# Performance work log

Hardware: AMD Instinct MI355X
Metric: run time of the kernel (lower is better)

Reference implementation:

```python
import jax, jax.numpy as jnp
import numpy as np

FT = 0.2  # clip floor (init arg ft)

def _norm_mat(m):
    # matrix / (count of nonzeros along last dim + 1e-30)
    deg = jnp.sum(m != 0, axis=-1, keepdims=True).astype(m.dtype)
    return m / (deg + 1e-30)

def _l2n(x):
    return x / (jnp.linalg.norm(x, axis=-1, keepdims=True) + 1e-30)

def setup_inputs():
    B, L, D, H, O = 2, 2048, 64, 64, 128
    N = 2 * L
    ks = jax.random.split(jax.random.key(0), 30)
    u = lambda i, s: jax.random.uniform(ks[i], s, jnp.float32)
    g = lambda i, s: jax.random.normal(ks[i], s, jnp.float32) * 0.05
    inp = {}
    inp['word_outputs_0'] = g(0, (B, L, D))
    inp['word_outputs_1'] = g(1, (B, L, D))
    inp['node_hidden'] = g(2, (B, D))
    inp['op_embedding'] = g(3, (B, O, D))
    inp['word_exist_sequence'] = (u(4, (B, N)) < 0.8).astype(jnp.float32)
    inp['word_exist_matrix'] = (u(5, (B, N, N)) < 0.8).astype(jnp.float32)
    inp['word_operator'] = (u(6, (B, N, O)) < 0.02).astype(jnp.float32)
    inp['word_word'] = (u(7, (B, N, N)) < 0.01).astype(jnp.float32)
    inp['depend_0'] = (u(8, (B, L, L)) < 0.05).astype(jnp.float32)
    inp['depend_1'] = (u(9, (B, L, L)) < 0.05).astype(jnp.float32)
    inp['goal_word'] = u(10, (B, N))
    names = [('Wg', (D, H)), ('bg', (H,)), ('Wwk', (D, H)), ('bwk', (H,)),
             ('Wws', (D, H)), ('bws', (H,)), ('Wo', (D, D)), ('bo', (D,)),
             ('Wupd', (3 * H, D)), ('bupd', (D,)), ('Wf', (3 * H + D, D)), ('bf', (D,)),
             ('Wf2', (2 * D, D)), ('bf2', (D,)), ('Wout', (D, D)), ('bout', (D,))]
    for i, (nm, s) in enumerate(names):
        inp[nm] = g(11 + i, s)
    return inp

def _forward(w0, w1, nh, opE, wes, wem, wop, ww, d0, d1, gw,
             Wg, bg, Wwk, bwk, Wws, bws, Wo, bo, Wupd, bupd, Wf, bf, Wf2, bf2, Wout, bout):
    all_w = jnp.concatenate([w0, w1], axis=1)                      # [B,N,D]
    goal_trans = (nh @ Wg + bg)[:, None, :]                        # [B,1,H] (broadcast = expand)
    word_g = _l2n(goal_trans * gw[..., None])                      # [B,N,H]
    word_w_k = _l2n(jnp.matmul(_norm_mat(ww * wem), all_w @ Wwk + bwk))
    ws0 = jnp.matmul(_norm_mat(d0), w0 @ Wws + bws)
    ws1 = jnp.matmul(_norm_mat(d1), w1 @ Wws + bws)
    word_w_s = _l2n(jnp.concatenate([ws0, ws1], axis=1))           # [B,N,H]
    neigh = jnp.concatenate([word_g, word_w_k, word_w_s], axis=-1)  # [B,N,3H]
    forget = jax.nn.sigmoid(jnp.concatenate([all_w, word_g, word_w_k, word_w_s], axis=-1) @ Wf + bf)
    word_updated = jnp.maximum(forget, FT) * all_w + (1.0 - forget) * jax.nn.relu(neigh @ Wupd + bupd)
    adj_op = _norm_mat(jnp.swapaxes(wes[..., None] * wop, 1, 2))   # [B,O,N]
    word_op = jnp.matmul(adj_op, word_updated @ Wo + bo)           # [B,O,D]
    forget2 = jax.nn.sigmoid(jnp.concatenate([opE, word_op], axis=-1) @ Wf2 + bf2)
    op_out = jnp.maximum(forget2, FT) * opE + (1.0 - forget2) * jax.nn.relu(word_op @ Wout + bout)
    # original returns (split(word_updated), op_embedding); concat along node axis here
    return jnp.concatenate([word_updated, op_out], axis=1)         # [B,N+O,D]

def reference(word_outputs_0, word_outputs_1, node_hidden, op_embedding,
              word_exist_sequence, word_exist_matrix, word_operator, word_word,
              depend_0, depend_1, goal_word,
              Wg, bg, Wwk, bwk, Wws, bws, Wo, bo, Wupd, bupd, Wf, bf, Wf2, bf2, Wout, bout):
    return _forward(word_outputs_0, word_outputs_1, node_hidden, op_embedding,
                    word_exist_sequence, word_exist_matrix, word_operator, word_word,
                    depend_0, depend_1, goal_word,
                    Wg, bg, Wwk, bwk, Wws, bws, Wo, bo, Wupd, bupd, Wf, bf, Wf2, bf2, Wout, bout)
```

## Files before the change

### kernel.cpp

```cpp
#include <hip/hip_runtime.h>
#include <cstdint>

typedef unsigned short u16;
typedef unsigned long long u64;

__device__ __forceinline__ float b2f(u16 u){
  union { uint32_t i; float f; } v; v.i = ((uint32_t)u) << 16; return v.f;
}
__device__ __forceinline__ u16 f2b(float f){
  union { float f; uint32_t i; } v; v.f = f;
  uint32_t r = v.i + 0x7FFFu + ((v.i >> 16) & 1u);
  return (u16)(r >> 16);
}
__device__ __forceinline__ float sigmoidf(float x){ return 1.0f / (1.0f + __expf(-x)); }
__device__ __forceinline__ uint32_t slot(uint4 v, int s){
  return (s==0) ? v.x : (s==1) ? v.y : (s==2) ? v.z : v.w;
}

__global__ void k_pre(const float* __restrict__ nh, const float* __restrict__ Wg,
                      const float* __restrict__ bg, float* __restrict__ ghat){
  int b = threadIdx.x >> 6, h = threadIdx.x & 63;
  float g = bg[h];
  for (int d = 0; d < 64; ++d) g += nh[b*64 + d] * Wg[d*64 + h];
  float ss = g * g;
  #pragma unroll
  for (int o = 32; o > 0; o >>= 1) ss += __shfl_xor(ss, o, 64);
  ghat[b*64 + h] = g / (sqrtf(ss) + 1e-30f);
}

__global__ __launch_bounds__(256) void k_xform(
    const float* __restrict__ w0, const float* __restrict__ w1,
    const float* __restrict__ Wwk, const float* __restrict__ bwk,
    const float* __restrict__ Wws, const float* __restrict__ bws,
    float* __restrict__ Xk, float* __restrict__ Xs){
  __shared__ float sWk[4096], sWs[4096];
  int tid = threadIdx.x;
  for (int i = tid; i < 1024; i += 256){
    ((float4*)sWk)[i] = ((const float4*)Wwk)[i];
    ((float4*)sWs)[i] = ((const float4*)Wws)[i];
  }
  __syncthreads();
  int lane = tid & 63, wave = tid >> 6;
  float bk = bwk[lane], bs = bws[lane];
  float aw[4];
  #pragma unroll
  for (int t = 0; t < 4; ++t){
    int row = blockIdx.x*4 + wave + t*2048;
    int b = row >> 12, n = row & 4095;
    aw[t] = (n < 2048) ? w0[((size_t)(b*2048 + n))*64 + lane]
                       : w1[((size_t)(b*2048 + n - 2048))*64 + lane];
  }
  #pragma unroll
  for (int t = 0; t < 4; ++t){
    int row = blockIdx.x*4 + wave + t*2048;
    float xk = bk, xs = bs;
    #pragma unroll 8
    for (int d = 0; d < 64; ++d){
      float a = __shfl(aw[t], d, 64);
      xk += a * sWk[d*64 + lane];
      xs += a * sWs[d*64 + lane];
    }
    Xk[(size_t)row*64 + lane] = xk;
    Xs[(size_t)row*64 + lane] = xs;
  }
}

template<bool TWO, int WPR>
__global__ __launch_bounds__(256) void k_maskmean(
    const float* __restrict__ mA, const float* __restrict__ mB,
    const float* __restrict__ X, float* __restrict__ outp,
    int rows, int cols, int xB, int xoff, int outB){
  __shared__ int q[4][1024];
  __shared__ float sacc[4][64];
  __shared__ int scnt[4];
  constexpr int RPB = 4 / WPR;
  int lane = threadIdx.x & 63, wave = threadIdx.x >> 6;
  int wir = wave & (WPR - 1), sub = wave / WPR;
  int rr = blockIdx.x * RPB + sub;
  int b = rr / rows, r = rr - b*rows;
  size_t base = ((size_t)b*rows + r) * cols + (size_t)wir*1024;
  const float* Xb = X + (size_t)b*xB + (size_t)xoff*64 + lane;
  uint4 av[4], bv[4];
  #pragma unroll
  for (int c = 0; c < 4; ++c){
    av[c] = ((const uint4*)(mA + base))[c*64 + lane];
    if (TWO) bv[c] = ((const uint4*)(mB + base))[c*64 + lane];
  }
  u64 lt = (1ULL << lane) - 1ULL;
  int cnt = 0;
  #pragma unroll
  for (int c = 0; c < 4; ++c){
    #pragma unroll
    for (int s = 0; s < 4; ++s){
      bool nz = (slot(av[c], s) & 0x7fffffffu) != 0;
      if (TWO) nz = nz && ((slot(bv[c], s) & 0x7fffffffu) != 0);
      u64 m = __ballot(nz);
      if (nz) q[wave][cnt + (int)__popcll(m & lt)] = wir*1024 + c*256 + lane*4 + s;
      cnt += (int)__popcll(m);
    }
  }
  float acc = 0.f;
  int i = 0;
  for (; i + 8 <= cnt; i += 8){
    int4 c0 = *(const int4*)&q[wave][i];
    int4 c1 = *(const int4*)&q[wave][i + 4];
    float v0 = Xb[(size_t)c0.x*64], v1 = Xb[(size_t)c0.y*64];
    float v2 = Xb[(size_t)c0.z*64], v3 = Xb[(size_t)c0.w*64];
    float v4 = Xb[(size_t)c1.x*64], v5 = Xb[(size_t)c1.y*64];
    float v6 = Xb[(size_t)c1.z*64], v7 = Xb[(size_t)c1.w*64];
    acc += ((v0 + v1) + (v2 + v3)) + ((v4 + v5) + (v6 + v7));
  }
  for (; i < cnt; ++i) acc += Xb[(size_t)q[wave][i]*64];
  sacc[wave][lane] = acc;
  if (lane == 0) scnt[wave] = cnt;
  __syncthreads();
  if (wir == 0){
    float t = 0.f; int dg = 0;
    #pragma unroll
    for (int j = 0; j < WPR; ++j){ t += sacc[sub*WPR + j][lane]; dg += scnt[sub*WPR + j]; }
    float mean = t / ((float)dg + 1e-30f);
    float ss = mean * mean;
    #pragma unroll
    for (int o = 32; o > 0; o >>= 1) ss += __shfl_xor(ss, o, 64);
    outp[(size_t)b*outB + (size_t)r*64 + lane] = mean / (sqrtf(ss) + 1e-30f);
  }
}

__global__ __launch_bounds__(256, 2) void k_update(
    const float* __restrict__ w0, const float* __restrict__ w1,
    const float* __restrict__ gw, const float* __restrict__ ghat,
    const float* __restrict__ wwkn, const float* __restrict__ wwsn,
    const float* __restrict__ Wf, const float* __restrict__ bf,
    const float* __restrict__ Wupd, const float* __restrict__ bupd,
    float* __restrict__ out, float* __restrict__ WU){
  __shared__ uint32_t pWf[128*64];
  __shared__ uint32_t pWu[96*64];
  __shared__ float xsh[4][256];
  int tid = threadIdx.x;
  for (int i = tid; i < 8192; i += 256){
    int k2 = i >> 6, ln = i & 63;
    pWf[i] = (uint32_t)f2b(Wf[(2*k2)*64 + ln]) | ((uint32_t)f2b(Wf[(2*k2+1)*64 + ln]) << 16);
  }
  for (int i = tid; i < 6144; i += 256){
    int k2 = i >> 6, ln = i & 63;
    pWu[i] = (uint32_t)f2b(Wupd[(2*k2)*64 + ln]) | ((uint32_t)f2b(Wupd[(2*k2+1)*64 + ln]) << 16);
  }
  __syncthreads();
  int lane = tid & 63, wave = tid >> 6;
  float bff = bf[lane], bup = bupd[lane];
  float aw[4], wgv[4], wk[4], wsv[4];
  #pragma unroll
  for (int t = 0; t < 4; ++t){
    int row = blockIdx.x*4 + wave + t*2048;
    int b = row >> 12, n = row & 4095;
    aw[t] = (n < 2048) ? w0[((size_t)(b*2048 + n))*64 + lane]
                       : w1[((size_t)(b*2048 + n - 2048))*64 + lane];
    float gvv = gw[b*4096 + n];
    wgv[t] = (gvv != 0.f) ? ghat[b*64 + lane] : 0.f;
    wk[t]  = wwkn[(size_t)row*64 + lane];
    wsv[t] = wwsn[(size_t)row*64 + lane];
  }
  #pragma unroll
  for (int t = 0; t < 4; ++t){
    int row = blockIdx.x*4 + wave + t*2048;
    int b = row >> 12, n = row & 4095;
    xsh[wave][lane] = aw[t]; xsh[wave][64 + lane] = wgv[t];
    xsh[wave][128 + lane] = wk[t]; xsh[wave][192 + lane] = wsv[t];
    float f = bff, u = bup;
    #pragma unroll 8
    for (int k2 = 0; k2 < 32; ++k2){
      float2 xv = *(const float2*)&xsh[wave][2*k2];
      uint32_t wf = pWf[k2*64 + lane];
      f += xv.x * b2f((u16)wf) + xv.y * b2f((u16)(wf >> 16));
    }
    #pragma unroll 8
    for (int k2 = 32; k2 < 128; ++k2){
      float2 xv = *(const float2*)&xsh[wave][2*k2];
      uint32_t wf = pWf[k2*64 + lane];
      uint32_t wu = pWu[(k2 - 32)*64 + lane];
      f += xv.x * b2f((u16)wf) + xv.y * b2f((u16)(wf >> 16));
      u += xv.x * b2f((u16)wu) + xv.y * b2f((u16)(wu >> 16));
    }
    f = sigmoidf(f);
    u = fmaxf(u, 0.f);
    float wu = fmaxf(f, 0.2f) * aw[t] + (1.f - f) * u;
    out[((size_t)b*4224 + n)*64 + lane] = wu;
    WU[(size_t)row*64 + lane] = wu;
  }
}

__global__ __launch_bounds__(256) void k_wuo(
    const float* __restrict__ WU, const float* __restrict__ Wo,
    const float* __restrict__ bo, float* __restrict__ WUo){
  __shared__ float sWo[4096];
  int tid = threadIdx.x;
  for (int i = tid; i < 1024; i += 256) ((float4*)sWo)[i] = ((const float4*)Wo)[i];
  __syncthreads();
  int lane = tid & 63, wave = tid >> 6;
  float boo = bo[lane];
  float wu[4];
  #pragma unroll
  for (int t = 0; t < 4; ++t){
    int row = blockIdx.x*4 + wave + t*2048;
    wu[t] = WU[(size_t)row*64 + lane];
  }
  #pragma unroll
  for (int t = 0; t < 4; ++t){
    int row = blockIdx.x*4 + wave + t*2048;
    float o = boo;
    #pragma unroll 8
    for (int d = 0; d < 64; ++d) o += __shfl(wu[t], d, 64) * sWo[d*64 + lane];
    WUo[(size_t)row*64 + lane] = o;
  }
}

__global__ __launch_bounds__(256) void k_opagg(
    const float* __restrict__ wes, const float* __restrict__ wop,
    const float* __restrict__ WUo, float* __restrict__ wordop){
  __shared__ int q[4][1024];
  __shared__ float sacc[4][64];
  __shared__ int scnt[4];
  int blk = blockIdx.x;
  int b = blk >> 7, o = blk & 127;
  int lane = threadIdx.x & 63, wave = threadIdx.x >> 6;
  const float* wesb = wes + b*4096 + wave*1024;
  const float* Xb = WUo + (size_t)b*4096*64 + lane;
  uint4 av[4]; float wv[16];
  #pragma unroll
  for (int c = 0; c < 4; ++c) av[c] = ((const uint4*)wesb)[c*64 + lane];
  #pragma unroll
  for (int c = 0; c < 4; ++c)
    #pragma unroll
    for (int s = 0; s < 4; ++s)
      wv[c*4 + s] = wop[(size_t)(b*4096 + wave*1024 + c*256 + lane*4 + s)*128 + o];
  u64 lt = (1ULL << lane) - 1ULL;
  int cnt = 0;
  #pragma unroll
  for (int c = 0; c < 4; ++c){
    #pragma unroll
    for (int s = 0; s < 4; ++s){
      bool nz = ((slot(av[c], s) & 0x7fffffffu) != 0) && (wv[c*4 + s] != 0.f);
      u64 m = __ballot(nz);
      if (nz) q[wave][cnt + (int)__popcll(m & lt)] = wave*1024 + c*256 + lane*4 + s;
      cnt += (int)__popcll(m);
    }
  }
  float acc = 0.f;
  int i = 0;
  for (; i + 8 <= cnt; i += 8){
    int4 c0 = *(const int4*)&q[wave][i];
    int4 c1 = *(const int4*)&q[wave][i + 4];
    float v0 = Xb[(size_t)c0.x*64], v1 = Xb[(size_t)c0.y*64];
    float v2 = Xb[(size_t)c0.z*64], v3 = Xb[(size_t)c0.w*64];
    float v4 = Xb[(size_t)c1.x*64], v5 = Xb[(size_t)c1.y*64];
    float v6 = Xb[(size_t)c1.z*64], v7 = Xb[(size_t)c1.w*64];
    acc += ((v0 + v1) + (v2 + v3)) + ((v4 + v5) + (v6 + v7));
  }
  for (; i < cnt; ++i) acc += Xb[(size_t)q[wave][i]*64];
  sacc[wave][lane] = acc;
  if (lane == 0) scnt[wave] = cnt;
  __syncthreads();
  if (wave == 0){
    float t = sacc[0][lane] + sacc[1][lane] + sacc[2][lane] + sacc[3][lane];
    float deg = (float)(scnt[0] + scnt[1] + scnt[2] + scnt[3]);
    wordop[(size_t)blk*64 + lane] = t / (deg + 1e-30f);
  }
}

__global__ __launch_bounds__(256) void k_opout(
    const float* __restrict__ opE, const float* __restrict__ wordop,
    const float* __restrict__ Wf2, const float* __restrict__ bf2,
    const float* __restrict__ Wout, const float* __restrict__ bout,
    float* __restrict__ out){
  __shared__ float sW2[8192];
  __shared__ float sWo[4096];
  __shared__ float xsh[4][128];
  int tid = threadIdx.x;
  for (int i = tid; i < 2048; i += 256) ((float4*)sW2)[i] = ((const float4*)Wf2)[i];
  for (int i = tid; i < 1024; i += 256) ((float4*)sWo)[i] = ((const float4*)Wout)[i];
  __syncthreads();
  int lane = tid & 63, wave = tid >> 6;
  int row = blockIdx.x*4 + wave;
  int b = row >> 7, o = row & 127;
  float e  = opE[(size_t)row*64 + lane];
  float wo = wordop[(size_t)row*64 + lane];
  xsh[wave][lane] = e; xsh[wave][64 + lane] = wo;
  float f = bf2[lane], u = bout[lane];
  #pragma unroll 8
  for (int k = 0; k < 128; ++k) f += xsh[wave][k] * sW2[k*64 + lane];
  #pragma unroll 8
  for (int d = 0; d < 64; ++d)  u += xsh[wave][64 + d] * sWo[d*64 + lane];
  f = sigmoidf(f);
  u = fmaxf(u, 0.f);
  float res = fmaxf(f, 0.2f) * e + (1.f - f) * u;
  out[((size_t)b*4224 + 4096 + o)*64 + lane] = res;
}

extern "C" void kernel_launch(void* const* d_in, const int* in_sizes, int n_in,
                              void* d_out, int out_size, void* d_ws, size_t ws_size,
                              hipStream_t stream){
  const float* w0   = (const float*)d_in[0];
  const float* w1   = (const float*)d_in[1];
  const float* nh   = (const float*)d_in[2];
  const float* opE  = (const float*)d_in[3];
  const float* wes  = (const float*)d_in[4];
  const float* wem  = (const float*)d_in[5];
  const float* wop  = (const float*)d_in[6];
  const float* ww   = (const float*)d_in[7];
  const float* d0   = (const float*)d_in[8];
  const float* d1   = (const float*)d_in[9];
  const float* gw   = (const float*)d_in[10];
  const float* Wg   = (const float*)d_in[11];
  const float* bg   = (const float*)d_in[12];
  const float* Wwk  = (const float*)d_in[13];
  const float* bwk  = (const float*)d_in[14];
  const float* Wws  = (const float*)d_in[15];
  const float* bws  = (const float*)d_in[16];
  const float* Wo   = (const float*)d_in[17];
  const float* bo   = (const float*)d_in[18];
  const float* Wupd = (const float*)d_in[19];
  const float* bupd = (const float*)d_in[20];
  const float* Wf   = (const float*)d_in[21];
  const float* bf   = (const float*)d_in[22];
  const float* Wf2  = (const float*)d_in[23];
  const float* bf2  = (const float*)d_in[24];
  const float* Wout = (const float*)d_in[25];
  const float* bout = (const float*)d_in[26];

  float* ws   = (float*)d_ws;
  float* ghat = ws;
  float* Xk   = ghat + 128;
  float* Xs   = Xk + 524288;
  float* wwkn = Xs + 524288;
  float* wwsn = wwkn + 524288;
  float* wopm = wwsn + 524288;
  float* WU   = Xk;
  float* WUo  = Xs;
  float* out  = (float*)d_out;

  k_pre<<<1, 128, 0, stream>>>(nh, Wg, bg, ghat);
  k_xform<<<512, 256, 0, stream>>>(w0, w1, Wwk, bwk, Wws, bws, Xk, Xs);
  k_maskmean<true , 4><<<8192, 256, 0, stream>>>(ww, wem, Xk, wwkn, 4096, 4096, 4096*64, 0,    4096*64);
  k_maskmean<false, 2><<<2048, 256, 0, stream>>>(d0, nullptr, Xs, wwsn,           2048, 2048, 4096*64, 0,    4096*64);
  k_maskmean<false, 2><<<2048, 256, 0, stream>>>(d1, nullptr, Xs, wwsn + 2048*64, 2048, 2048, 4096*64, 2048, 4096*64);
  k_update<<<512, 256, 0, stream>>>(w0, w1, gw, ghat, wwkn, wwsn, Wf, bf, Wupd, bupd, out, WU);
  k_wuo<<<512, 256, 0, stream>>>(WU, Wo, bo, WUo);
  k_opagg<<<256, 256, 0, stream>>>(wes, wop, WUo, wopm);
  k_opout<<<64, 256, 0, stream>>>(opE, wopm, Wf2, bf2, Wout, bout, out);
}
```

Before: 454.2 us.

## Replace sparse gather mask-mean with dense bf16 MFMA split-K matmul

The ballot/compaction plus gather mask-mean kernels are replaced by a dense matmul. Mask nonzeros become bf16 ones and are multiplied by a transposed bf16 copy of the transformed features using MFMA 16x16x32 instructions, with double-buffered LDS staging, split-K and atomicAdd reduction. A separate kernel then L2-normalizes the sums, which removes the need to divide by the degree. The intent is to turn latency-bound irregular gathers into a streaming, tensor-core-friendly pass. The cost is bf16 rounding of the features, extra transpose and memset launches, and atomic traffic.

```diff
diff --git a/kernel.cpp b/kernel.cpp
--- a/kernel.cpp
+++ b/kernel.cpp
@@ -3,18 +3,20 @@
 
 typedef unsigned short u16;
 typedef unsigned long long u64;
-
-__device__ __forceinline__ float b2f(u16 u){
-  union { uint32_t i; float f; } v; v.i = ((uint32_t)u) << 16; return v.f;
-}
+typedef __attribute__((ext_vector_type(8))) short bf16x8;
+typedef __attribute__((ext_vector_type(4))) float f32x4;
+
 __device__ __forceinline__ u16 f2b(float f){
   union { float f; uint32_t i; } v; v.f = f;
   uint32_t r = v.i + 0x7FFFu + ((v.i >> 16) & 1u);
   return (u16)(r >> 16);
 }
+__device__ __forceinline__ float b2f(u16 u){
+  union { uint32_t i; float f; } v; v.i = ((uint32_t)u) << 16; return v.f;
+}
 __device__ __forceinline__ float sigmoidf(float x){ return 1.0f / (1.0f + __expf(-x)); }
-__device__ __forceinline__ uint32_t slot(uint4 v, int s){
-  return (s==0) ? v.x : (s==1) ? v.y : (s==2) ? v.z : v.w;
+__device__ __forceinline__ uint32_t nzb(float a){
+  return (__float_as_uint(a) << 1) ? 0x3F80u : 0u;
 }
 
 __global__ void k_pre(const float* __restrict__ nh, const float* __restrict__ Wg,
@@ -65,65 +67,123 @@
   }
 }
 
-template<bool TWO, int WPR>
-__global__ __launch_bounds__(256) void k_maskmean(
-    const float* __restrict__ mA, const float* __restrict__ mB,
-    const float* __restrict__ X, float* __restrict__ outp,
-    int rows, int cols, int xB, int xoff, int outB){
-  __shared__ int q[4][1024];
-  __shared__ float sacc[4][64];
-  __shared__ int scnt[4];
-  constexpr int RPB = 4 / WPR;
-  int lane = threadIdx.x & 63, wave = threadIdx.x >> 6;
-  int wir = wave & (WPR - 1), sub = wave / WPR;
-  int rr = blockIdx.x * RPB + sub;
-  int b = rr / rows, r = rr - b*rows;
-  size_t base = ((size_t)b*rows + r) * cols + (size_t)wir*1024;
-  const float* Xb = X + (size_t)b*xB + (size_t)xoff*64 + lane;
-  uint4 av[4], bv[4];
+__global__ __launch_bounds__(256) void k_tr(const float* __restrict__ src, u16* __restrict__ dst){
+  __shared__ u16 sm[64][65];
+  int tile = blockIdx.x;
+  int b = tile >> 6, n0 = (tile & 63) * 64;
+  int tid = threadIdx.x;
+  int r = tid >> 2, seg = (tid & 3) * 16;
+  const float* s = src + ((size_t)b*4096 + n0 + r) * 64 + seg;
   #pragma unroll
   for (int c = 0; c < 4; ++c){
-    av[c] = ((const uint4*)(mA + base))[c*64 + lane];
-    if (TWO) bv[c] = ((const uint4*)(mB + base))[c*64 + lane];
-  }
-  u64 lt = (1ULL << lane) - 1ULL;
-  int cnt = 0;
-  #pragma unroll
-  for (int c = 0; c < 4; ++c){
+    float4 v = ((const float4*)s)[c];
+    sm[r][seg + c*4 + 0] = f2b(v.x);
+    sm[r][seg + c*4 + 1] = f2b(v.y);
+    sm[r][seg + c*4 + 2] = f2b(v.z);
+    sm[r][seg + c*4 + 3] = f2b(v.w);
+  }
+  __syncthreads();
+  int d = tid >> 2, ns = (tid & 3) * 16;
+  u16* o = dst + (size_t)b*64*4096 + (size_t)d*4096 + n0 + ns;
+  #pragma unroll
+  for (int j = 0; j < 8; ++j){
+    uint32_t lo = sm[ns + 2*j][d], hi = sm[ns + 2*j + 1][d];
+    ((uint32_t*)o)[j] = lo | (hi << 16);
+  }
+}
+
+template<bool TWO>
+__global__ __launch_bounds__(256) void k_mm(
+    const float* __restrict__ M1, const float* __restrict__ M2,
+    const u16* __restrict__ XT, float* __restrict__ sums,
+    int rowsPB, int cols, int numRT, int kspan, int xoff){
+  __shared__ u16 Bm[2][64*72];
+  __shared__ u16 Ax[2][64*72];
+  int rt = blockIdx.x % numRT;
+  int ks = blockIdx.x / numRT;
+  int rr0 = rt * 64;
+  int b = rr0 / rowsPB, r0 = rr0 % rowsPB;
+  int k0 = ks * kspan;
+  int tid = threadIdx.x;
+  int rsub = tid >> 2, seg = tid & 3, kk = seg * 16;
+  const float* m1t = M1 + ((size_t)b*rowsPB + r0 + rsub) * cols + k0 + kk;
+  const float* m2t = TWO ? (M2 + ((size_t)b*rowsPB + r0 + rsub) * cols + k0 + kk) : nullptr;
+  const u16*   xtt = XT + (size_t)b*64*4096 + (size_t)rsub*4096 + xoff + k0 + kk;
+  int lane = tid & 63, w = tid >> 6, quad = lane >> 4, l15 = lane & 15;
+
+  f32x4 acc[4] = {f32x4{0,0,0,0}, f32x4{0,0,0,0}, f32x4{0,0,0,0}, f32x4{0,0,0,0}};
+  int niter = kspan >> 6;
+
+  float4 am0, am1, am2, am3, bn0, bn1, bn2, bn3;
+  uint4 x0, x1;
+
+#define ISSUE(IT) do{ size_t off = (size_t)(IT) * 64;                         \
+    am0 = ((const float4*)(m1t + off))[0]; am1 = ((const float4*)(m1t + off))[1]; \
+    am2 = ((const float4*)(m1t + off))[2]; am3 = ((const float4*)(m1t + off))[3]; \
+    if (TWO){                                                                  \
+      bn0 = ((const float4*)(m2t + off))[0]; bn1 = ((const float4*)(m2t + off))[1]; \
+      bn2 = ((const float4*)(m2t + off))[2]; bn3 = ((const float4*)(m2t + off))[3]; \
+    }                                                                          \
+    x0 = ((const uint4*)(xtt + off))[0]; x1 = ((const uint4*)(xtt + off))[1]; }while(0)
+
+#define PK(a, bb) (TWO ? ((nzb(a.x) && nzb(bb.x) ? 0x3F80u : 0u) | ((nzb(a.y) && nzb(bb.y) ? 0x3F80u : 0u) << 16)) \
+                       : (nzb(a.x) | (nzb(a.y) << 16)))
+#define PK2(a, bb) (TWO ? ((nzb(a.z) && nzb(bb.z) ? 0x3F80u : 0u) | ((nzb(a.w) && nzb(bb.w) ? 0x3F80u : 0u) << 16)) \
+                        : (nzb(a.z) | (nzb(a.w) << 16)))
+
+#define COMMIT(BUF) do{                                                        \
+    uint4 pa, pb;                                                              \
+    pa.x = PK(am0, bn0); pa.y = PK2(am0, bn0); pa.z = PK(am1, bn1); pa.w = PK2(am1, bn1); \
+    pb.x = PK(am2, bn2); pb.y = PK2(am2, bn2); pb.z = PK(am3, bn3); pb.w = PK2(am3, bn3); \
+    *(uint4*)&Bm[BUF][rsub*72 + kk]     = pa;                                  \
+    *(uint4*)&Bm[BUF][rsub*72 + kk + 8] = pb;                                  \
+    *(uint4*)&Ax[BUF][rsub*72 + kk]     = x0;                                  \
+    *(uint4*)&Ax[BUF][rsub*72 + kk + 8] = x1; }while(0)
+
+  ISSUE(0);
+  COMMIT(0);
+  __syncthreads();
+  for (int it = 0; it < niter; ++it){
+    int buf = it & 1;
+    if (it + 1 < niter) ISSUE(it + 1);
     #pragma unroll
-    for (int s = 0; s < 4; ++s){
-      bool nz = (slot(av[c], s) & 0x7fffffffu) != 0;
-      if (TWO) nz = nz && ((slot(bv[c], s) & 0x7fffffffu) != 0);
-      u64 m = __ballot(nz);
-      if (nz) q[wave][cnt + (int)__popcll(m & lt)] = wir*1024 + c*256 + lane*4 + s;
-      cnt += (int)__popcll(m);
+    for (int s = 0; s < 2; ++s){
+      int ko = s*32 + quad*8;
+      bf16x8 bfr = *(const bf16x8*)&Bm[buf][(w*16 + l15)*72 + ko];
+      #pragma unroll
+      for (int m = 0; m < 4; ++m){
+        bf16x8 afr = *(const bf16x8*)&Ax[buf][(m*16 + l15)*72 + ko];
+        acc[m] = __builtin_amdgcn_mfma_f32_16x16x32_bf16(afr, bfr, acc[m], 0, 0, 0);
+      }
     }
-  }
-  float acc = 0.f;
-  int i = 0;
-  for (; i + 8 <= cnt; i += 8){
-    int4 c0 = *(const int4*)&q[wave][i];
-    int4 c1 = *(const int4*)&q[wave][i + 4];
-    float v0 = Xb[(size_t)c0.x*64], v1 = Xb[(size_t)c0.y*64];
-    float v2 = Xb[(size_t)c0.z*64], v3 = Xb[(size_t)c0.w*64];
-    float v4 = Xb[(size_t)c1.x*64], v5 = Xb[(size_t)c1.y*64];
-    float v6 = Xb[(size_t)c1.z*64], v7 = Xb[(size_t)c1.w*64];
-    acc += ((v0 + v1) + (v2 + v3)) + ((v4 + v5) + (v6 + v7));
-  }
-  for (; i < cnt; ++i) acc += Xb[(size_t)q[wave][i]*64];
-  sacc[wave][lane] = acc;
-  if (lane == 0) scnt[wave] = cnt;
-  __syncthreads();
-  if (wir == 0){
-    float t = 0.f; int dg = 0;
+    if (it + 1 < niter) COMMIT((it + 1) & 1);
+    __syncthreads();
+  }
+  float* od = sums + (size_t)(b*4096 + xoff + r0 + w*16 + l15) * 64;
+  #pragma unroll
+  for (int m = 0; m < 4; ++m)
     #pragma unroll
-    for (int j = 0; j < WPR; ++j){ t += sacc[sub*WPR + j][lane]; dg += scnt[sub*WPR + j]; }
-    float mean = t / ((float)dg + 1e-30f);
-    float ss = mean * mean;
-    #pragma unroll
-    for (int o = 32; o > 0; o >>= 1) ss += __shfl_xor(ss, o, 64);
-    outp[(size_t)b*outB + (size_t)r*64 + lane] = mean / (sqrtf(ss) + 1e-30f);
-  }
+    for (int g = 0; g < 4; ++g)
+      atomicAdd(&od[m*16 + quad*4 + g], acc[m][g]);
+#undef ISSUE
+#undef COMMIT
+#undef PK
+#undef PK2
+}
+
+__global__ __launch_bounds__(256) void k_norm(
+    const float* __restrict__ sb, const float* __restrict__ sd,
+    float* __restrict__ wwkn, float* __restrict__ wwsn){
+  int idx = blockIdx.x*4 + (threadIdx.x >> 6);
+  int lane = threadIdx.x & 63;
+  const float* s; float* d;
+  if (idx < 8192){ s = sb + (size_t)idx*64; d = wwkn + (size_t)idx*64; }
+  else           { s = sd + (size_t)(idx - 8192)*64; d = wwsn + (size_t)(idx - 8192)*64; }
+  float v = s[lane];
+  float ss = v * v;
+  #pragma unroll
+  for (int o = 32; o > 0; o >>= 1) ss += __shfl_xor(ss, o, 64);
+  d[lane] = v / (sqrtf(ss) + 1e-30f);
 }
 
 __global__ __launch_bounds__(256, 2) void k_update(
@@ -239,7 +299,8 @@
   for (int c = 0; c < 4; ++c){
     #pragma unroll
     for (int s = 0; s < 4; ++s){
-      bool nz = ((slot(av[c], s) & 0x7fffffffu) != 0) && (wv[c*4 + s] != 0.f);
+      uint32_t wa = (s==0)?av[c].x:(s==1)?av[c].y:(s==2)?av[c].z:av[c].w;
+      bool nz = ((wa & 0x7fffffffu) != 0) && (wv[c*4 + s] != 0.f);
       u64 m = __ballot(nz);
       if (nz) q[wave][cnt + (int)__popcll(m & lt)] = wave*1024 + c*256 + lane*4 + s;
       cnt += (int)__popcll(m);
@@ -334,15 +395,24 @@
   float* wwkn = Xs + 524288;
   float* wwsn = wwkn + 524288;
   float* wopm = wwsn + 524288;
+  u16*  XkT   = (u16*)(wopm + 16384);
+  u16*  XsT   = (u16*)(wopm + 16384 + 262144);
+  float* sums_big = Xk;
+  float* sums_dep = Xs;
   float* WU   = Xk;
   float* WUo  = Xs;
   float* out  = (float*)d_out;
 
   k_pre<<<1, 128, 0, stream>>>(nh, Wg, bg, ghat);
   k_xform<<<512, 256, 0, stream>>>(w0, w1, Wwk, bwk, Wws, bws, Xk, Xs);
-  k_maskmean<true , 4><<<8192, 256, 0, stream>>>(ww, wem, Xk, wwkn, 4096, 4096, 4096*64, 0,    4096*64);
-  k_maskmean<false, 2><<<2048, 256, 0, stream>>>(d0, nullptr, Xs, wwsn,           2048, 2048, 4096*64, 0,    4096*64);
-  k_maskmean<false, 2><<<2048, 256, 0, stream>>>(d1, nullptr, Xs, wwsn + 2048*64, 2048, 2048, 4096*64, 2048, 4096*64);
+  k_tr<<<128, 256, 0, stream>>>(Xk, XkT);
+  k_tr<<<128, 256, 0, stream>>>(Xs, XsT);
+  hipMemsetAsync(sums_big, 0, 524288 * sizeof(float), stream);
+  hipMemsetAsync(sums_dep, 0, 524288 * sizeof(float), stream);
+  k_mm<true ><<<1024, 256, 0, stream>>>(ww, wem, XkT, sums_big, 4096, 4096, 128, 512, 0);
+  k_mm<false><<<256, 256, 0, stream>>>(d0, nullptr, XsT, sums_dep, 2048, 2048, 64, 512, 0);
+  k_mm<false><<<256, 256, 0, stream>>>(d1, nullptr, XsT, sums_dep, 2048, 2048, 64, 512, 2048);
+  k_norm<<<4096, 256, 0, stream>>>(sums_big, sums_dep, wwkn, wwsn);
   k_update<<<512, 256, 0, stream>>>(w0, w1, gw, ghat, wwkn, wwsn, Wf, bf, Wupd, bupd, out, WU);
   k_wuo<<<512, 256, 0, stream>>>(WU, Wo, bo, WUo);
   k_opagg<<<256, 256, 0, stream>>>(wes, wop, WUo, wopm);
```

Result: slower. 519.8 us (+14.5%).

## Precompute adjacency bitmasks, then gather with prefix-sum compaction and bf16 outputs

Applied to the files above, without the earlier changes.

The fused mask-and-mean kernels are split in two. A streaming pass packs each adjacency row, and the word-operator mask, into 64-bit bitmasks via ballots. A second pass expands the set bits with a wave prefix-sum into index lists and gathers the transformed rows. The operator aggregation reads compact per-node bitmasks instead of striding down the word_operator column, which is meant to remove heavily uncoalesced reads. The normalized neighbour means are now stored as bf16, which lowers precision and adds extra kernel launches and bitmask traffic.

```diff
diff --git a/kernel.cpp b/kernel.cpp
--- a/kernel.cpp
+++ b/kernel.cpp
@@ -4,18 +4,15 @@
 typedef unsigned short u16;
 typedef unsigned long long u64;
 
-__device__ __forceinline__ float b2f(u16 u){
-  union { uint32_t i; float f; } v; v.i = ((uint32_t)u) << 16; return v.f;
-}
 __device__ __forceinline__ u16 f2b(float f){
   union { float f; uint32_t i; } v; v.f = f;
   uint32_t r = v.i + 0x7FFFu + ((v.i >> 16) & 1u);
   return (u16)(r >> 16);
 }
+__device__ __forceinline__ float b2f(u16 u){
+  union { uint32_t i; float f; } v; v.i = ((uint32_t)u) << 16; return v.f;
+}
 __device__ __forceinline__ float sigmoidf(float x){ return 1.0f / (1.0f + __expf(-x)); }
-__device__ __forceinline__ uint32_t slot(uint4 v, int s){
-  return (s==0) ? v.x : (s==1) ? v.y : (s==2) ? v.z : v.w;
-}
 
 __global__ void k_pre(const float* __restrict__ nh, const float* __restrict__ Wg,
                       const float* __restrict__ bg, float* __restrict__ ghat){
@@ -65,43 +62,77 @@
   }
 }
 
-template<bool TWO, int WPR>
-__global__ __launch_bounds__(256) void k_maskmean(
-    const float* __restrict__ mA, const float* __restrict__ mB,
-    const float* __restrict__ X, float* __restrict__ outp,
-    int rows, int cols, int xB, int xoff, int outB){
-  __shared__ int q[4][1024];
-  __shared__ float sacc[4][64];
-  __shared__ int scnt[4];
-  constexpr int RPB = 4 / WPR;
+template<bool TWO, int JS>
+__global__ __launch_bounds__(256) void k_bits(
+    const float* __restrict__ A, const float* __restrict__ B, u64* __restrict__ bits){
   int lane = threadIdx.x & 63, wave = threadIdx.x >> 6;
-  int wir = wave & (WPR - 1), sub = wave / WPR;
-  int rr = blockIdx.x * RPB + sub;
-  int b = rr / rows, r = rr - b*rows;
-  size_t base = ((size_t)b*rows + r) * cols + (size_t)wir*1024;
-  const float* Xb = X + (size_t)b*xB + (size_t)xoff*64 + lane;
-  uint4 av[4], bv[4];
-  #pragma unroll
-  for (int c = 0; c < 4; ++c){
-    av[c] = ((const uint4*)(mA + base))[c*64 + lane];
-    if (TWO) bv[c] = ((const uint4*)(mB + base))[c*64 + lane];
-  }
-  u64 lt = (1ULL << lane) - 1ULL;
-  int cnt = 0;
-  #pragma unroll
-  for (int c = 0; c < 4; ++c){
+  int row = blockIdx.x*4 + wave;
+  const float* a = A + (size_t)row * (JS*256) + lane*4;
+  const float* bb = TWO ? (B + (size_t)row * (JS*256) + lane*4) : nullptr;
+  u64 myword = 0;
+  #pragma unroll 4
+  for (int j = 0; j < JS; ++j){
+    float4 va = *(const float4*)(a + j*256);
+    float4 vb;
+    if (TWO) vb = *(const float4*)(bb + j*256);
     #pragma unroll
     for (int s = 0; s < 4; ++s){
-      bool nz = (slot(av[c], s) & 0x7fffffffu) != 0;
-      if (TWO) nz = nz && ((slot(bv[c], s) & 0x7fffffffu) != 0);
+      float x = (s==0)?va.x:(s==1)?va.y:(s==2)?va.z:va.w;
+      bool nz = (x != 0.f);
+      if (TWO){
+        float y = (s==0)?vb.x:(s==1)?vb.y:(s==2)?vb.z:vb.w;
+        nz = nz && (y != 0.f);
+      }
       u64 m = __ballot(nz);
-      if (nz) q[wave][cnt + (int)__popcll(m & lt)] = wir*1024 + c*256 + lane*4 + s;
-      cnt += (int)__popcll(m);
+      if (lane == j*4 + s) myword = m;
     }
   }
+  if (lane < JS*4) bits[(size_t)row*(JS*4) + lane] = myword;
+}
+
+__global__ __launch_bounds__(256) void k_bitsop(
+    const float* __restrict__ wes, const float* __restrict__ wop, u64* __restrict__ bitOp){
+  int lane = threadIdx.x & 63, wave = threadIdx.x >> 6;
+  int wg = blockIdx.x*4 + wave;
+  for (int it = 0; it < 16; ++it){
+    int ng = wg*16 + it;
+    float2 v = ((const float2*)(wop + (size_t)ng*128))[lane];
+    float e = wes[ng];
+    u64 m0 = __ballot(e != 0.f && v.x != 0.f);
+    u64 m1 = __ballot(e != 0.f && v.y != 0.f);
+    if (lane == 0) bitOp[(size_t)ng*2]     = m0;
+    if (lane == 1) bitOp[(size_t)ng*2 + 1] = m1;
+  }
+}
+
+__global__ __launch_bounds__(256) void k_gath(
+    const u64* __restrict__ bits, const float* __restrict__ X,
+    u16* __restrict__ outp, int rowsPB, int WPR, int xoff){
+  __shared__ int q[4][256];
+  int lane = threadIdx.x & 63, wave = threadIdx.x >> 6;
+  int rowIdx = blockIdx.x*4 + wave;
+  int b = rowIdx / rowsPB, r = rowIdx - b*rowsPB;
+  u64 word = (lane < WPR) ? bits[(size_t)rowIdx*WPR + lane] : 0ULL;
+  int c = __popcll(word);
+  int pre = c;
+  #pragma unroll
+  for (int off = 1; off < 64; off <<= 1){
+    int t = __shfl_up(pre, off, 64);
+    if (lane >= off) pre += t;
+  }
+  int total = __shfl(pre, 63, 64);
+  int base = pre - c;
+  int colhi = (lane >> 2) * 256 + (lane & 3);
+  u64 m = word;
+  while (m){
+    int p = __builtin_ctzll(m); m &= m - 1;
+    q[wave][base++] = colhi + p*4;
+  }
+  __syncthreads();
+  const float* Xb = X + ((size_t)b*4096 + xoff)*64 + lane;
   float acc = 0.f;
   int i = 0;
-  for (; i + 8 <= cnt; i += 8){
+  for (; i + 8 <= total; i += 8){
     int4 c0 = *(const int4*)&q[wave][i];
     int4 c1 = *(const int4*)&q[wave][i + 4];
     float v0 = Xb[(size_t)c0.x*64], v1 = Xb[(size_t)c0.y*64];
@@ -110,26 +141,17 @@
     float v6 = Xb[(size_t)c1.z*64], v7 = Xb[(size_t)c1.w*64];
     acc += ((v0 + v1) + (v2 + v3)) + ((v4 + v5) + (v6 + v7));
   }
-  for (; i < cnt; ++i) acc += Xb[(size_t)q[wave][i]*64];
-  sacc[wave][lane] = acc;
-  if (lane == 0) scnt[wave] = cnt;
-  __syncthreads();
-  if (wir == 0){
-    float t = 0.f; int dg = 0;
-    #pragma unroll
-    for (int j = 0; j < WPR; ++j){ t += sacc[sub*WPR + j][lane]; dg += scnt[sub*WPR + j]; }
-    float mean = t / ((float)dg + 1e-30f);
-    float ss = mean * mean;
-    #pragma unroll
-    for (int o = 32; o > 0; o >>= 1) ss += __shfl_xor(ss, o, 64);
-    outp[(size_t)b*outB + (size_t)r*64 + lane] = mean / (sqrtf(ss) + 1e-30f);
-  }
+  for (; i < total; ++i) acc += Xb[(size_t)q[wave][i]*64];
+  float ss = acc * acc;
+  #pragma unroll
+  for (int o = 32; o > 0; o >>= 1) ss += __shfl_xor(ss, o, 64);
+  outp[((size_t)b*4096 + xoff + r)*64 + lane] = f2b(acc / (sqrtf(ss) + 1e-30f));
 }
 
 __global__ __launch_bounds__(256, 2) void k_update(
     const float* __restrict__ w0, const float* __restrict__ w1,
     const float* __restrict__ gw, const float* __restrict__ ghat,
-    const float* __restrict__ wwkn, const float* __restrict__ wwsn,
+    const u16* __restrict__ wwkn, const u16* __restrict__ wwsn,
     const float* __restrict__ Wf, const float* __restrict__ bf,
     const float* __restrict__ Wupd, const float* __restrict__ bupd,
     float* __restrict__ out, float* __restrict__ WU){
@@ -157,8 +179,8 @@
                        : w1[((size_t)(b*2048 + n - 2048))*64 + lane];
     float gvv = gw[b*4096 + n];
     wgv[t] = (gvv != 0.f) ? ghat[b*64 + lane] : 0.f;
-    wk[t]  = wwkn[(size_t)row*64 + lane];
-    wsv[t] = wwsn[(size_t)row*64 + lane];
+    wk[t]  = b2f(wwkn[(size_t)row*64 + lane]);
+    wsv[t] = b2f(wwsn[(size_t)row*64 + lane]);
   }
   #pragma unroll
   for (int t = 0; t < 4; ++t){
@@ -215,36 +237,27 @@
 }
 
 __global__ __launch_bounds__(256) void k_opagg(
-    const float* __restrict__ wes, const float* __restrict__ wop,
-    const float* __restrict__ WUo, float* __restrict__ wordop){
-  __shared__ int q[4][1024];
-  __shared__ float sacc[4][64];
-  __shared__ int scnt[4];
-  int blk = blockIdx.x;
-  int b = blk >> 7, o = blk & 127;
+    const u64* __restrict__ bitOp, const float* __restrict__ WUo,
+    float* __restrict__ wordop){
+  __shared__ int q[4][256];
   int lane = threadIdx.x & 63, wave = threadIdx.x >> 6;
-  const float* wesb = wes + b*4096 + wave*1024;
-  const float* Xb = WUo + (size_t)b*4096*64 + lane;
-  uint4 av[4]; float wv[16];
-  #pragma unroll
-  for (int c = 0; c < 4; ++c) av[c] = ((const uint4*)wesb)[c*64 + lane];
-  #pragma unroll
-  for (int c = 0; c < 4; ++c)
-    #pragma unroll
-    for (int s = 0; s < 4; ++s)
-      wv[c*4 + s] = wop[(size_t)(b*4096 + wave*1024 + c*256 + lane*4 + s)*128 + o];
+  int rowIdx = blockIdx.x*4 + wave;
+  int b = rowIdx >> 7, o = rowIdx & 127;
+  int wrd = o & 1, bit = o >> 1;
+  const u64* bp = bitOp + (size_t)b*4096*2 + wrd;
   u64 lt = (1ULL << lane) - 1ULL;
   int cnt = 0;
-  #pragma unroll
-  for (int c = 0; c < 4; ++c){
-    #pragma unroll
-    for (int s = 0; s < 4; ++s){
-      bool nz = ((slot(av[c], s) & 0x7fffffffu) != 0) && (wv[c*4 + s] != 0.f);
-      u64 m = __ballot(nz);
-      if (nz) q[wave][cnt + (int)__popcll(m & lt)] = wave*1024 + c*256 + lane*4 + s;
-      cnt += (int)__popcll(m);
-    }
-  }
+  #pragma unroll 4
+  for (int it = 0; it < 64; ++it){
+    int n = it*64 + lane;
+    u64 v = bp[(size_t)n*2];
+    bool nz = (v >> bit) & 1ULL;
+    u64 m = __ballot(nz);
+    if (nz) q[wave][cnt + (int)__popcll(m & lt)] = n;
+    cnt += (int)__popcll(m);
+  }
+  __syncthreads();
+  const float* Xb = WUo + (size_t)b*4096*64 + lane;
   float acc = 0.f;
   int i = 0;
   for (; i + 8 <= cnt; i += 8){
@@ -257,14 +270,7 @@
     acc += ((v0 + v1) + (v2 + v3)) + ((v4 + v5) + (v6 + v7));
   }
   for (; i < cnt; ++i) acc += Xb[(size_t)q[wave][i]*64];
-  sacc[wave][lane] = acc;
-  if (lane == 0) scnt[wave] = cnt;
-  __syncthreads();
-  if (wave == 0){
-    float t = sacc[0][lane] + sacc[1][lane] + sacc[2][lane] + sacc[3][lane];
-    float deg = (float)(scnt[0] + scnt[1] + scnt[2] + scnt[3]);
-    wordop[(size_t)blk*64 + lane] = t / (deg + 1e-30f);
-  }
+  wordop[(size_t)rowIdx*64 + lane] = acc / ((float)cnt + 1e-30f);
 }
 
 __global__ __launch_bounds__(256) void k_opout(
@@ -329,22 +335,30 @@
 
   float* ws   = (float*)d_ws;
   float* ghat = ws;
-  float* Xk   = ghat + 128;
-  float* Xs   = Xk + 524288;
-  float* wwkn = Xs + 524288;
-  float* wwsn = wwkn + 524288;
-  float* wopm = wwsn + 524288;
+  float* Xk   = ws + 128;
+  float* Xs   = ws + 524416;
+  float* wopm = ws + 1048704;
+  u16*  wwkn  = (u16*)(ws + 1065088);
+  u16*  wwsn  = (u16*)(ws + 1327232);
+  u64*  bitBig= (u64*)(ws + 1589376);
+  u64*  bitD0 = (u64*)(ws + 2637952);
+  u64*  bitD1 = (u64*)(ws + 2900096);
+  u64*  bitOp = (u64*)(ws + 3162240);
   float* WU   = Xk;
   float* WUo  = Xs;
   float* out  = (float*)d_out;
 
   k_pre<<<1, 128, 0, stream>>>(nh, Wg, bg, ghat);
   k_xform<<<512, 256, 0, stream>>>(w0, w1, Wwk, bwk, Wws, bws, Xk, Xs);
-  k_maskmean<true , 4><<<8192, 256, 0, stream>>>(ww, wem, Xk, wwkn, 4096, 4096, 4096*64, 0,    4096*64);
-  k_maskmean<false, 2><<<2048, 256, 0, stream>>>(d0, nullptr, Xs, wwsn,           2048, 2048, 4096*64, 0,    4096*64);
-  k_maskmean<false, 2><<<2048, 256, 0, stream>>>(d1, nullptr, Xs, wwsn + 2048*64, 2048, 2048, 4096*64, 2048, 4096*64);
+  k_bits<true , 16><<<2048, 256, 0, stream>>>(ww, wem, bitBig);
+  k_bits<false, 8 ><<<1024, 256, 0, stream>>>(d0, nullptr, bitD0);
+  k_bits<false, 8 ><<<1024, 256, 0, stream>>>(d1, nullptr, bitD1);
+  k_bitsop<<<128, 256, 0, stream>>>(wes, wop, bitOp);
+  k_gath<<<2048, 256, 0, stream>>>(bitBig, Xk, wwkn, 4096, 64, 0);
+  k_gath<<<1024, 256, 0, stream>>>(bitD0, Xs, wwsn, 2048, 32, 0);
+  k_gath<<<1024, 256, 0, stream>>>(bitD1, Xs, wwsn, 2048, 32, 2048);
   k_update<<<512, 256, 0, stream>>>(w0, w1, gw, ghat, wwkn, wwsn, Wf, bf, Wupd, bupd, out, WU);
   k_wuo<<<512, 256, 0, stream>>>(WU, Wo, bo, WUo);
-  k_opagg<<<256, 256, 0, stream>>>(wes, wop, WUo, wopm);
+  k_opagg<<<64, 256, 0, stream>>>(bitOp, WUo, wopm);
   k_opout<<<64, 256, 0, stream>>>(opE, wopm, Wf2, bf2, Wout, bout, out);
 }
```

Result: slower. 507.4 us (+11.7%).
